# Kernel optimization log

Measured on AMD Instinct MI355X. Metric: run time of the kernel, lower is better.

The kernel has to match this reference:

```python
import jax, jax.numpy as jnp
import numpy as np

B, N, M = 8, 4096, 4096


def setup_inputs() -> dict:
    key = jax.random.key(0)
    k1, k2 = jax.random.split(key)
    tar = jax.random.normal(k1, (B, N, 3), dtype=jnp.float32)
    src = jax.random.normal(k2, (B, M, 3), dtype=jnp.float32)
    return {"tar": tar, "src": src}


def reference(tar, src):
    # diff: [b, n, m, 3]; dist: [b, n, m] Euclidean norm
    diff = tar[:, :, None, :] - src[:, None, :, :]
    dist = jnp.sqrt(jnp.sum(diff * diff, axis=-1))
    # complete: for each target point, min over source points, mean over n -> [b]
    complete = jnp.mean(jnp.min(dist, axis=2), axis=1)
    # accuracy: for each source point, min over target points, mean over m -> [b]
    accuracy = jnp.mean(jnp.min(dist, axis=1), axis=1)
    # reduction='mean' over batch axis
    complete = jnp.mean(complete, axis=-1)
    accuracy = jnp.mean(accuracy, axis=-1)
    chamfer = 0.5 * (complete + accuracy)
    return (accuracy, complete, chamfer)
```

## Files before the change

### kernel.cpp

```cpp
#include <hip/hip_runtime.h>
#include <math.h>

#define B_ 8


__global__ __launch_bounds__(256) void init_ws_kernel(unsigned int* ws, int n) {
    int i = blockIdx.x * 256 + threadIdx.x;
    if (i < n) ws[i] = 0x7F800000u;
}

template <int QPT, int CHUNK>
__global__ __launch_bounds__(256) void minsq_kernel(
    const float* __restrict__ tar, const float* __restrict__ src,
    unsigned int* __restrict__ ws, int N, int M)
{
    const int z   = blockIdx.z;
    const int dir = (z >= B_) ? 1 : 0;
    const int b   = dir ? (z - B_) : z;
    const float* __restrict__ qry = dir ? src : tar;
    const float* __restrict__ pts = dir ? tar : src;
    const int K = dir ? M : N;
    const int L = dir ? N : M;
    unsigned int* __restrict__ out =
        ws + (dir ? (size_t)B_ * N : (size_t)0) + (size_t)b * K;

    const int base = blockIdx.y * CHUNK;
    if (base >= L) return;
    const int cnt = min(CHUNK, L - base);

    __shared__ float4 sp[CHUNK];
    const float* __restrict__ psrc = pts + ((size_t)b * L + base) * 3;
    const int t = threadIdx.x;
    for (int i = t; i < cnt; i += 256) {
        float px = psrc[3 * i + 0];
        float py = psrc[3 * i + 1];
        float pz = psrc[3 * i + 2];
        sp[i] = make_float4(px, py, pz, fmaf(px, px, fmaf(py, py, pz * pz)));
    }
    __syncthreads();

    const int qbase = blockIdx.x * (256 * QPT);
    float qx2[QPT], qy2[QPT], qz2[QPT], qw[QPT], mn[QPT];
#pragma unroll
    for (int k = 0; k < QPT; ++k) {
        int qi = qbase + k * 256 + t;
        if (qi < K) {
            const float* qp = qry + ((size_t)b * K + qi) * 3;
            float x = qp[0], y = qp[1], zc = qp[2];
            qx2[k] = -2.f * x; qy2[k] = -2.f * y; qz2[k] = -2.f * zc;
            qw[k] = fmaf(x, x, fmaf(y, y, zc * zc));
        } else {
            qx2[k] = 0.f; qy2[k] = 0.f; qz2[k] = 0.f; qw[k] = 0.f;
        }
        mn[k] = 3.4e38f;
    }

    if (cnt == CHUNK) {
#pragma unroll 4
        for (int j = 0; j < CHUNK; j += 2) {
            float4 p0 = sp[j];
            float4 p1 = sp[j + 1];
#pragma unroll
            for (int k = 0; k < QPT; ++k) {
                float d0 = fmaf(qx2[k], p0.x,
                           fmaf(qy2[k], p0.y,
                           fmaf(qz2[k], p0.z, p0.w)));
                float d1 = fmaf(qx2[k], p1.x,
                           fmaf(qy2[k], p1.y,
                           fmaf(qz2[k], p1.z, p1.w)));
                mn[k] = fminf(mn[k], fminf(d0, d1));
            }
        }
    } else {
        int j = 0;
        for (; j + 1 < cnt; j += 2) {
            float4 p0 = sp[j];
            float4 p1 = sp[j + 1];
#pragma unroll
            for (int k = 0; k < QPT; ++k) {
                float d0 = fmaf(qx2[k], p0.x,
                           fmaf(qy2[k], p0.y,
                           fmaf(qz2[k], p0.z, p0.w)));
                float d1 = fmaf(qx2[k], p1.x,
                           fmaf(qy2[k], p1.y,
                           fmaf(qz2[k], p1.z, p1.w)));
                mn[k] = fminf(mn[k], fminf(d0, d1));
            }
        }
        if (j < cnt) {
            float4 p0 = sp[j];
#pragma unroll
            for (int k = 0; k < QPT; ++k) {
                float d0 = fmaf(qx2[k], p0.x,
                           fmaf(qy2[k], p0.y,
                           fmaf(qz2[k], p0.z, p0.w)));
                mn[k] = fminf(mn[k], d0);
            }
        }
    }

#pragma unroll
    for (int k = 0; k < QPT; ++k) {
        int qi = qbase + k * 256 + t;
        if (qi < K) {
            float d2 = fmaxf(mn[k] + qw[k], 0.f);
            atomicMin(&out[qi], __float_as_uint(d2));
        }
    }
}

__global__ __launch_bounds__(256) void reduce1_kernel(
    const unsigned int* __restrict__ ws, float* __restrict__ partials,
    int N, int M)
{
    const int nt = B_ * N;
    const int ns = B_ * M;
    const int gid = blockIdx.x * 256 + threadIdx.x;
    const int stride = gridDim.x * 256;
    float s_t = 0.f, s_s = 0.f;
    for (int i = gid; i < nt; i += stride) s_t += sqrtf(__uint_as_float(ws[i]));
    for (int i = gid; i < ns; i += stride) s_s += sqrtf(__uint_as_float(ws[nt + i]));

#pragma unroll
    for (int off = 32; off > 0; off >>= 1) {
        s_t += __shfl_down(s_t, off);
        s_s += __shfl_down(s_s, off);
    }
    __shared__ float rt[4], rs[4];
    const int wid = threadIdx.x >> 6, lid = threadIdx.x & 63;
    if (lid == 0) { rt[wid] = s_t; rs[wid] = s_s; }
    __syncthreads();
    if (threadIdx.x == 0) {
        float a = rt[0] + rt[1] + rt[2] + rt[3];
        float c = rs[0] + rs[1] + rs[2] + rs[3];
        partials[blockIdx.x]       = a;
        partials[128 + blockIdx.x] = c;
    }
}

__global__ __launch_bounds__(128) void finalize_kernel(
    const float* __restrict__ partials, float* __restrict__ outp, int N, int M)
{
    const int t = threadIdx.x;
    float s_t = partials[t];
    float s_s = partials[128 + t];
#pragma unroll
    for (int off = 32; off > 0; off >>= 1) {
        s_t += __shfl_down(s_t, off);
        s_s += __shfl_down(s_s, off);
    }
    __shared__ float rt[2], rs[2];
    if ((t & 63) == 0) { rt[t >> 6] = s_t; rs[t >> 6] = s_s; }
    __syncthreads();
    if (t == 0) {
        float complete = (rt[0] + rt[1]) / (float)(B_ * N);
        float accuracy = (rs[0] + rs[1]) / (float)(B_ * M);
        outp[0] = accuracy;
        outp[1] = complete;
        outp[2] = 0.5f * (accuracy + complete);
    }
}

extern "C" void kernel_launch(void* const* d_in, const int* in_sizes, int n_in,
                              void* d_out, int out_size, void* d_ws, size_t ws_size,
                              hipStream_t stream) {
    const float* tar = (const float*)d_in[0];
    const float* src = (const float*)d_in[1];
    const int N = in_sizes[0] / (B_ * 3);
    const int M = in_sizes[1] / (B_ * 3);
    unsigned int* ws = (unsigned int*)d_ws;
    float* partials = (float*)(ws + (size_t)B_ * (N + M));

    const int tot = B_ * (N + M);
    init_ws_kernel<<<dim3((tot + 255) / 256), dim3(256), 0, stream>>>(ws, tot);

    constexpr int QPT = 4, CHUNK = 512;
    const int KL = (N > M) ? N : M;
    const int gx = (KL + 256 * QPT - 1) / (256 * QPT);
    const int gy = (KL + CHUNK - 1) / CHUNK;
    dim3 grid(gx, gy, 2 * B_);
    minsq_kernel<QPT, CHUNK><<<grid, dim3(256), 0, stream>>>(tar, src, ws, N, M);

    reduce1_kernel<<<dim3(128), dim3(256), 0, stream>>>(ws, partials, N, M);
    finalize_kernel<<<dim3(1), dim3(128), 0, stream>>>(partials, (float*)d_out, N, M);
}
```

Measured before the change: 85.50 us.

## Replace atomicMin workspace with per-chunk partial-min slabs reduced in one pass

Each source chunk now writes its per-query minima to its own workspace slab with plain stores instead of doing atomicMin into a shared array, which removes the init kernel and atomic contention. The reduction kernel takes the min across all slabs, then sums the square roots and accumulates the final means into the output with atomicAdd, which replaces the separate finalize kernel (the output is zeroed with a memset). The cost is a workspace eight times larger, more global traffic in the reduction, and float atomicAdd ordering that makes the summation order nondeterministic.

Result: slower. 91.35 us (+6.8%).

```diff
diff --git a/kernel.cpp b/kernel.cpp
--- a/kernel.cpp
+++ b/kernel.cpp
@@ -4,15 +4,10 @@
 #define B_ 8
 
 
-__global__ __launch_bounds__(256) void init_ws_kernel(unsigned int* ws, int n) {
-    int i = blockIdx.x * 256 + threadIdx.x;
-    if (i < n) ws[i] = 0x7F800000u;
-}
-
 template <int QPT, int CHUNK>
 __global__ __launch_bounds__(256) void minsq_kernel(
     const float* __restrict__ tar, const float* __restrict__ src,
-    unsigned int* __restrict__ ws, int N, int M)
+    float* __restrict__ ws, int N, int M)
 {
     const int z   = blockIdx.z;
     const int dir = (z >= B_) ? 1 : 0;
@@ -21,12 +16,15 @@
     const float* __restrict__ pts = dir ? tar : src;
     const int K = dir ? M : N;
     const int L = dir ? N : M;
-    unsigned int* __restrict__ out =
-        ws + (dir ? (size_t)B_ * N : (size_t)0) + (size_t)b * K;
 
     const int base = blockIdx.y * CHUNK;
     if (base >= L) return;
     const int cnt = min(CHUNK, L - base);
+
+    const size_t slabStride = (size_t)B_ * (N + M);
+    float* __restrict__ out = ws + (size_t)blockIdx.y * slabStride
+                                 + (dir ? (size_t)B_ * N : (size_t)0)
+                                 + (size_t)b * K;
 
     __shared__ float4 sp[CHUNK];
     const float* __restrict__ psrc = pts + ((size_t)b * L + base) * 3;
@@ -103,23 +101,36 @@
     for (int k = 0; k < QPT; ++k) {
         int qi = qbase + k * 256 + t;
         if (qi < K) {
-            float d2 = fmaxf(mn[k] + qw[k], 0.f);
-            atomicMin(&out[qi], __float_as_uint(d2));
+            out[qi] = fmaxf(mn[k] + qw[k], 0.f);
         }
     }
 }
 
-__global__ __launch_bounds__(256) void reduce1_kernel(
-    const unsigned int* __restrict__ ws, float* __restrict__ partials,
-    int N, int M)
+template <int CHUNK>
+__global__ __launch_bounds__(256) void reduce_kernel(
+    const float* __restrict__ ws, float* __restrict__ outp, int N, int M)
 {
     const int nt = B_ * N;
     const int ns = B_ * M;
+    const size_t slabStride = (size_t)B_ * (N + M);
+    const int nslab0 = (M + CHUNK - 1) / CHUNK;
+    const int nslab1 = (N + CHUNK - 1) / CHUNK;
+
     const int gid = blockIdx.x * 256 + threadIdx.x;
     const int stride = gridDim.x * 256;
+
     float s_t = 0.f, s_s = 0.f;
-    for (int i = gid; i < nt; i += stride) s_t += sqrtf(__uint_as_float(ws[i]));
-    for (int i = gid; i < ns; i += stride) s_s += sqrtf(__uint_as_float(ws[nt + i]));
+    for (int i = gid; i < nt; i += stride) {
+        float m = ws[i];
+        for (int s = 1; s < nslab0; ++s) m = fminf(m, ws[s * slabStride + i]);
+        s_t += sqrtf(m);
+    }
+    for (int i = gid; i < ns; i += stride) {
+        const size_t off = (size_t)nt + i;
+        float m = ws[off];
+        for (int s = 1; s < nslab1; ++s) m = fminf(m, ws[s * slabStride + off]);
+        s_s += sqrtf(m);
+    }
 
 #pragma unroll
     for (int off = 32; off > 0; off >>= 1) {
@@ -131,33 +142,11 @@
     if (lid == 0) { rt[wid] = s_t; rs[wid] = s_s; }
     __syncthreads();
     if (threadIdx.x == 0) {
-        float a = rt[0] + rt[1] + rt[2] + rt[3];
-        float c = rs[0] + rs[1] + rs[2] + rs[3];
-        partials[blockIdx.x]       = a;
-        partials[128 + blockIdx.x] = c;
-    }
-}
-
-__global__ __launch_bounds__(128) void finalize_kernel(
-    const float* __restrict__ partials, float* __restrict__ outp, int N, int M)
-{
-    const int t = threadIdx.x;
-    float s_t = partials[t];
-    float s_s = partials[128 + t];
-#pragma unroll
-    for (int off = 32; off > 0; off >>= 1) {
-        s_t += __shfl_down(s_t, off);
-        s_s += __shfl_down(s_s, off);
-    }
-    __shared__ float rt[2], rs[2];
-    if ((t & 63) == 0) { rt[t >> 6] = s_t; rs[t >> 6] = s_s; }
-    __syncthreads();
-    if (t == 0) {
-        float complete = (rt[0] + rt[1]) / (float)(B_ * N);
-        float accuracy = (rs[0] + rs[1]) / (float)(B_ * M);
-        outp[0] = accuracy;
-        outp[1] = complete;
-        outp[2] = 0.5f * (accuracy + complete);
+        float ct = (rt[0] + rt[1] + rt[2] + rt[3]) / (float)nt;
+        float ac = (rs[0] + rs[1] + rs[2] + rs[3]) / (float)ns;
+        atomicAdd(&outp[0], ac);
+        atomicAdd(&outp[1], ct);
+        atomicAdd(&outp[2], 0.5f * (ac + ct));
     }
 }
 
@@ -168,11 +157,10 @@
     const float* src = (const float*)d_in[1];
     const int N = in_sizes[0] / (B_ * 3);
     const int M = in_sizes[1] / (B_ * 3);
-    unsigned int* ws = (unsigned int*)d_ws;
-    float* partials = (float*)(ws + (size_t)B_ * (N + M));
+    float* ws = (float*)d_ws;
+    float* outp = (float*)d_out;
 
-    const int tot = B_ * (N + M);
-    init_ws_kernel<<<dim3((tot + 255) / 256), dim3(256), 0, stream>>>(ws, tot);
+    hipMemsetAsync(outp, 0, (size_t)out_size * sizeof(float), stream);
 
     constexpr int QPT = 4, CHUNK = 512;
     const int KL = (N > M) ? N : M;
@@ -181,6 +169,5 @@
     dim3 grid(gx, gy, 2 * B_);
     minsq_kernel<QPT, CHUNK><<<grid, dim3(256), 0, stream>>>(tar, src, ws, N, M);
 
-    reduce1_kernel<<<dim3(128), dim3(256), 0, stream>>>(ws, partials, N, M);
-    finalize_kernel<<<dim3(1), dim3(128), 0, stream>>>(partials, (float*)d_out, N, M);
+    reduce_kernel<CHUNK><<<dim3(128), dim3(256), 0, stream>>>(ws, outp, N, M);
 }
```
